# Kernel optimization log

Hardware: AMD Instinct MI355X
Metric: run time of the kernel (lower is better)

The kernel has to match this reference:

```python
import jax, jax.numpy as jnp
import numpy as np

N, E, F, FE, L = 12000, 120000, 768, 64, 16
Z = 2 * F + F  # concat(x_i, x_j, e) width = 2304


def setup_inputs() -> dict:
    key = jax.random.key(0)
    ks = jax.random.split(key, 24)
    s = 0.02

    def w(k, shape):
        return jax.random.normal(k, shape, dtype=jnp.float32) * s

    inp = {
        "x": jax.random.normal(ks[0], (N, F), dtype=jnp.float32),
        "e_raw": jax.random.normal(ks[1], (E, FE), dtype=jnp.float32),
        "src": jax.random.randint(ks[2], (E,), 0, N, dtype=jnp.int32),
        "dst": jax.random.randint(ks[3], (E,), 0, N, dtype=jnp.int32),
        "W_pre": w(ks[4], (FE, F)), "b_pre": jnp.zeros((F,), jnp.float32),
        "Wf1": w(ks[5], (Z, F)), "bf1": jnp.zeros((F,), jnp.float32),
        "Ws1": w(ks[6], (Z, F)), "bs1": jnp.zeros((F,), jnp.float32),
        "We1": w(ks[7], (Z, F)), "be1": jnp.zeros((F,), jnp.float32),
        "Wf2": w(ks[8], (Z, F)), "bf2": jnp.zeros((F,), jnp.float32),
        "Ws2": w(ks[9], (Z, F)), "bs2": jnp.zeros((F,), jnp.float32),
        "We2": w(ks[10], (Z, F)), "be2": jnp.zeros((F,), jnp.float32),
        "Wd": w(ks[11], (F, L)), "bd": jnp.zeros((L,), jnp.float32),
    }
    return inp


def _crystal_conv(x, e, src, dst, Wf, bf, Ws, bs, We, be):
    # z_ij = x_i || x_j || e_ij  (targets=dst, sources=src, Spektral convention)
    z = jnp.concatenate([x[dst], x[src], e], axis=-1)  # [E, 2304]
    msg = jax.nn.relu(z @ Ws + bs) * jax.nn.sigmoid(z @ Wf + bf)  # [E, F]
    gate = jax.nn.sigmoid(z @ We + be)  # [E, F] (stored as conv.e)
    agg = jax.ops.segment_sum(msg, dst, num_segments=N)  # scatter-sum to targets
    return x + agg, gate


def reference(x, e_raw, src, dst, W_pre, b_pre, Wf1, bf1, Ws1, bs1, We1, be1,
              Wf2, bf2, Ws2, bs2, We2, be2, Wd, bd):
    e = jnp.tanh(e_raw @ W_pre + b_pre)  # pre_edge Dense(768, tanh)
    # dropout layers are identity at inference
    x1, g1 = _crystal_conv(x, e, src, dst, Wf1, bf1, Ws1, bs1, We1, be1)
    e = e + e * g1
    x2, g2 = _crystal_conv(x1, e, src, dst, Wf2, bf2, Ws2, bs2, We2, be2)
    pooled = jnp.sum(x2, axis=0, keepdims=True)  # GlobalSumPool -> [1, F]
    return jax.nn.softmax(pooled @ Wd + bd, axis=-1)  # [1, n_labels]
```

## Files before the change

kernel.cpp:

```cpp
#include <hip/hip_runtime.h>
#include <stdint.h>

#define EN 120000
#define NN 12000
#define FF 768

typedef __attribute__((ext_vector_type(8))) short short8;
typedef __attribute__((ext_vector_type(4))) float floatx4;
typedef __attribute__((ext_vector_type(2))) float floatx2;
typedef __attribute__((ext_vector_type(2))) long long2v;

#ifdef __has_builtin
#if __has_builtin(__builtin_amdgcn_cvt_pk_f32_fp8) && __has_builtin(__builtin_amdgcn_cvt_f32_fp8)
#define HAS_HW_FP8 1
#endif
#if __has_builtin(__builtin_amdgcn_cvt_pk_fp8_f32)
#define HAS_HW_FP8E 1
#endif
#endif
#ifndef HAS_HW_FP8
#define HAS_HW_FP8 0
#endif
#ifndef HAS_HW_FP8E
#define HAS_HW_FP8E 0
#endif

__device__ __forceinline__ short f2b(float f) {
  union { float f; uint32_t i; } v; v.f = f;
  uint32_t r = (v.i + 0x7fffu + ((v.i >> 16) & 1u)) >> 16;
  return (short)(uint16_t)r;
}
__device__ __forceinline__ float f8tof(uint32_t b) {
  union { uint32_t i; float f; } u;
  u.i = (b & 0x7f) << 20;
  float v = u.f * 0x1p120f;
  return (b & 0x80) ? -v : v;
}
__device__ __forceinline__ uint8_t ftof8(float v) {
#if HAS_HW_FP8E
  return (uint8_t)(__builtin_amdgcn_cvt_pk_fp8_f32(v, v, 0, false) & 0xff);
#else
  union { float f; uint32_t i; } u;
  u.f = fabsf(v) * 0x1p-120f;
  uint32_t r = (u.i + 0x7ffffu + ((u.i >> 20) & 1u)) >> 20;
  if (r > 0x7eu) r = 0x7eu;
  return (uint8_t)(r | ((v < 0.f) ? 0x80u : 0u));
#endif
}
__device__ __forceinline__ floatx2 f8pair(uint32_t u) {
#if HAS_HW_FP8
  return __builtin_amdgcn_cvt_pk_f32_fp8(u, false);
#else
  floatx2 r; r.x = f8tof(u & 0xff); r.y = f8tof((u >> 8) & 0xff); return r;
#endif
}
__device__ __forceinline__ floatx2 f8pair_hi(uint32_t u) {
#if HAS_HW_FP8
  return __builtin_amdgcn_cvt_pk_f32_fp8(u, true);
#else
  floatx2 r; r.x = f8tof((u >> 16) & 0xff); r.y = f8tof((u >> 24) & 0xff); return r;
#endif
}
__device__ __forceinline__ float f8one(uint32_t u) {
#if HAS_HW_FP8
  return __builtin_amdgcn_cvt_f32_fp8(u, 0);
#else
  return f8tof(u & 0xff);
#endif
}
__device__ __forceinline__ float sigm(float x) { return 1.f / (1.f + __expf(-x)); }
__device__ __forceinline__ float tanh_fast(float x) {
  float ax = fabsf(x);
  float t = __expf(-2.f * ax);
  float r = (1.f - t) / (1.f + t);
  return copysignf(r, x);
}
__device__ __forceinline__ void async_ld16(const void* g, void* l) {
  __builtin_amdgcn_global_load_lds(
      (const __attribute__((address_space(1))) void*)g,
      (__attribute__((address_space(3))) void*)l, 16, 0, 0);
}
__device__ __forceinline__ int permk(int n) {
  return (n & ~63) | (((n >> 3) & 3) << 4) | (((n >> 5) & 1) << 3) | (n & 7);
}

template <int NW, int EPI, int F8AB>
__global__ __launch_bounds__(256, 2) void gemm_fused(
    const char* __restrict__ A, int lda,
    const char* __restrict__ Bt, int ldb, int wstride,
    int M, int K,
    void* __restrict__ outP, int ldout,
    const float* __restrict__ bias0, const float* __restrict__ bias1,
    const float* __restrict__ bias2,
    const int* __restrict__ dst, const int* __restrict__ src,
    const uint8_t* __restrict__ Pn, int pstride,
    const uint8_t* __restrict__ eInF8, uint8_t* __restrict__ e2Out,
    float* __restrict__ agg)
{
  __shared__ alignas(16) char lA[64 * 64];
  __shared__ alignas(16) char lB[NW * 128 * 64];

  const int tid  = threadIdx.x;
  const int wave = tid >> 6;
  const int lane = tid & 63;
  const int quad = lane >> 4;
  const int l16  = lane & 15;

  const int gx  = gridDim.x;
  const int nwg = gx * gridDim.y;
  int flat = blockIdx.y * gx + blockIdx.x;
  {
    const int q = nwg >> 3, r = nwg & 7;
    const int xcd = flat & 7, lid = flat >> 3;
    flat = (xcd < r ? xcd * (q + 1) : r * (q + 1) + (xcd - r) * q) + lid;
  }
  const int mBase = (flat / gx) * 64;
  const int nBase = (flat % gx) * 128;

  floatx4 acc[NW][4][2];
#pragma unroll
  for (int w = 0; w < NW; ++w)
#pragma unroll
    for (int mt = 0; mt < 4; ++mt)
#pragma unroll
      for (int nt = 0; nt < 2; ++nt)
#pragma unroll
        for (int r = 0; r < 4; ++r) acc[w][mt][nt][r] = 0.f;

  int i4 = tid >> 2;
  int am = mBase + ((i4 & 12) << 2) + ((i4 >> 4) << 2) + (i4 & 3);
  if (am > M - 1) am = M - 1;
  const char* aSrc = A + (size_t)am * lda + (tid & 3) * 16;

  const char* bSrc[NW * 2];
#pragma unroll
  for (int i = 0; i < NW * 2; ++i) {
    int t2 = tid + i * 256;
    int w  = t2 >> 9;
    int r  = (t2 >> 2) & 127;
    bSrc[i] = Bt + (size_t)w * wstride + (size_t)(nBase + r) * ldb + (t2 & 3) * 16;
  }

  const int Kb = K * (F8AB ? 1 : 2);

  for (int k0 = 0; k0 < Kb; k0 += 64) {
    __syncthreads();
    async_ld16(aSrc + k0, lA + tid * 16);
#pragma unroll
    for (int i = 0; i < NW * 2; ++i)
      async_ld16(bSrc[i] + k0, lB + (tid + i * 256) * 16);
    __syncthreads();

    if constexpr (F8AB) {
      long2v av[4];
#pragma unroll
      for (int mt = 0; mt < 4; ++mt)
        av[mt] = *(const long2v*)(lA + (mt * 16 + l16) * 64 + quad * 16);
#pragma unroll
      for (int w = 0; w < NW; ++w)
#pragma unroll
        for (int nt = 0; nt < 2; ++nt) {
          long2v bv = *(const long2v*)(lB + (w * 128 + wave * 32 + nt * 16 + l16) * 64 + quad * 16);
#pragma unroll
          for (int mt = 0; mt < 4; ++mt) {
            acc[w][mt][nt] = __builtin_amdgcn_mfma_f32_16x16x32_fp8_fp8(
                av[mt].x, bv.x, acc[w][mt][nt], 0, 0, 0);
            acc[w][mt][nt] = __builtin_amdgcn_mfma_f32_16x16x32_fp8_fp8(
                av[mt].y, bv.y, acc[w][mt][nt], 0, 0, 0);
          }
        }
    } else {
      short8 af[4];
#pragma unroll
      for (int mt = 0; mt < 4; ++mt)
        af[mt] = *(const short8*)(lA + (mt * 16 + l16) * 64 + quad * 16);
#pragma unroll
      for (int w = 0; w < NW; ++w)
#pragma unroll
        for (int nt = 0; nt < 2; ++nt) {
          short8 bf = *(const short8*)(lB + (w * 128 + wave * 32 + nt * 16 + l16) * 64 + quad * 16);
#pragma unroll
          for (int mt = 0; mt < 4; ++mt)
            acc[w][mt][nt] = __builtin_amdgcn_mfma_f32_16x16x32_bf16(
                af[mt], bf, acc[w][mt][nt], 0, 0, 0);
        }
    }
  }

  const int colW = nBase + wave * 32;

  float bb0[2], bb1[2], bb2[2];
  if (EPI == 1 || EPI == 2 || EPI == 3) {
#pragma unroll
    for (int nt = 0; nt < 2; ++nt) {
      int n = colW + nt * 16 + l16;
      bb0[nt] = bias0[n];
      if (EPI == 2 || EPI == 3) bb1[nt] = bias1[n];
      if (EPI == 2) bb2[nt] = bias2[n];
    }
  }

  if constexpr (EPI == 2 || EPI == 3) {
    const int n0 = colW + l16;
    const int pOff = ((n0 >> 5) << 6) + ((n0 & 15) << 2);
    const int eOff = ((n0 >> 5) << 5) + ((n0 & 15) << 1);
    const int pk0 = permk(n0), pk1 = permk(n0 + 16);
    const int mQ = mBase + quad * 16;
    int dp = -1;
    float run0 = 0.f, run1 = 0.f;
    float fd0 = 0.f, fd1 = 0.f, sd0 = 0.f, sd1 = 0.f, ed0 = 0.f, ed1 = 0.f;
#pragma unroll
    for (int j = 0; j < 16; ++j) {
      const int mt = j >> 2, r = j & 3;
      const int m = mQ + j;
      const int d = dst[m];
      const int s = src[m];
      if (d != dp) {
        if (dp >= 0) {
          atomicAdd(&agg[(size_t)dp * FF + n0], run0);
          atomicAdd(&agg[(size_t)dp * FF + n0 + 16], run1);
        }
        run0 = 0.f; run1 = 0.f; dp = d;
        const uint8_t* Pd = Pn + (size_t)d * pstride;
        uint32_t td = *(const uint32_t*)(Pd + pOff);
        floatx2 ta = f8pair(td), tb = f8pair_hi(td);
        fd0 = ta.x + bb0[0]; sd0 = ta.y + bb1[0];
        fd1 = tb.x + bb0[1]; sd1 = tb.y + bb1[1];
        if (EPI == 2) {
          uint32_t te = *(const unsigned short*)(Pd + 3072 + eOff);
          floatx2 ea = f8pair(te);
          ed0 = ea.x + bb2[0]; ed1 = ea.y + bb2[1];
        }
      }
      const uint8_t* Ps = Pn + (size_t)s * pstride;
      uint32_t tm = *(const uint32_t*)(Ps + 1536 + pOff);
      floatx2 ma = f8pair(tm), mb = f8pair_hi(tm);
      float hf0 = acc[0][mt][0][r] + ma.x + fd0;
      float hs0 = acc[1][mt][0][r] + ma.y + sd0;
      float hf1 = acc[0][mt][1][r] + mb.x + fd1;
      float hs1 = acc[1][mt][1][r] + mb.y + sd1;
      run0 += fmaxf(hs0, 0.f) * sigm(hf0);
      run1 += fmaxf(hs1, 0.f) * sigm(hf1);
      if (EPI == 2) {
        uint32_t me = *(const unsigned short*)(Ps + 3840 + eOff);
        floatx2 ea = f8pair(me);
        float he0 = acc[2][mt][0][r] + ea.x + ed0;
        float he1 = acc[2][mt][1][r] + ea.y + ed1;
        float ev0 = f8one(eInF8[(size_t)m * FF + pk0]);
        float ev1 = f8one(eInF8[(size_t)m * FF + pk1]);
        e2Out[(size_t)m * FF + pk0] = ftof8(ev0 * (1.f + sigm(he0)));
        e2Out[(size_t)m * FF + pk1] = ftof8(ev1 * (1.f + sigm(he1)));
      }
    }
    if (dp >= 0) {
      atomicAdd(&agg[(size_t)dp * FF + n0], run0);
      atomicAdd(&agg[(size_t)dp * FF + n0 + 16], run1);
    }
  } else {
#pragma unroll
    for (int mt = 0; mt < 4; ++mt) {
#pragma unroll
      for (int r = 0; r < 4; ++r) {
        int m = mBase + quad * 16 + mt * 4 + r;
        if (m >= M) continue;
#pragma unroll
        for (int nt = 0; nt < 2; ++nt) {
          int n = colW + nt * 16 + l16;
          float v0 = acc[0][mt][nt][r];
          if (EPI == 0) {
            int q = n / 768, j = n - q * 768;
            int h = (j >> 4) & 1;
            size_t o;
            if (q < 4)
              o = (size_t)(((q & 1) ? 1536 : 0) + ((j >> 5) << 6) + ((j & 15) << 2)
                           + (h << 1) + ((q >> 1) & 1));
            else
              o = (size_t)((q == 4 ? 3072 : 3840) + ((j >> 5) << 5) + ((j & 15) << 1) + h);
            ((uint8_t*)outP)[(size_t)m * ldout + o] = ftof8(v0);
          } else {
            ((uint8_t*)outP)[(size_t)m * ldout + permk(n)] = ftof8(tanh_fast(v0 + bb0[nt]));
          }
        }
      }
    }
  }
}

__global__ void hist_k(const int* __restrict__ dst, int* __restrict__ cnt) {
  int i = blockIdx.x * 256 + threadIdx.x;
  if (i < EN) atomicAdd(&cnt[dst[i]], 1);
}

__global__ void scan_k(const int* __restrict__ cnt, int* __restrict__ off) {
  __shared__ int part[1024];
  int t = threadIdx.x;
  int base = t * 12;
  int loc[12];
  int s = 0;
#pragma unroll
  for (int j = 0; j < 12; ++j) {
    int idx = base + j;
    int c = idx < NN ? cnt[idx] : 0;
    loc[j] = s; s += c;
  }
  part[t] = s;
  __syncthreads();
  for (int d = 1; d < 1024; d <<= 1) {
    int v = (t >= d) ? part[t - d] : 0;
    __syncthreads();
    part[t] += v;
    __syncthreads();
  }
  int pre = (t == 0) ? 0 : part[t - 1];
#pragma unroll
  for (int j = 0; j < 12; ++j) {
    int idx = base + j;
    if (idx < NN) off[idx] = pre + loc[j];
  }
}

__global__ void scatter_k(const int* __restrict__ dst, int* __restrict__ off,
                          int* __restrict__ perm) {
  int i = blockIdx.x * 256 + threadIdx.x;
  if (i < EN) { int p = atomicAdd(&off[dst[i]], 1); perm[p] = i; }
}

__global__ void permute_k(const int* __restrict__ dst, const int* __restrict__ src,
                          const int* __restrict__ perm, int* __restrict__ dstS,
                          int* __restrict__ srcS) {
  int i = blockIdx.x * 256 + threadIdx.x;
  if (i < EN) { int e = perm[i]; dstS[i] = dst[e]; srcS[i] = src[e]; }
}

__global__ void gather_f2b(const float* __restrict__ e_raw, const int* __restrict__ perm,
                           short* __restrict__ out, int n) {
  int i = blockIdx.x * 256 + threadIdx.x;
  if (i < n) {
    int j = i >> 6, t = i & 63;
    out[i] = f2b(e_raw[(size_t)perm[j] * 64 + t]);
  }
}

__global__ void conv_f2f8(const float* __restrict__ in, uint8_t* __restrict__ out, int n) {
  int i = blockIdx.x * 256 + threadIdx.x;
  if (i < n) {
    int row = i / FF, col = i - row * FF;
    out[(size_t)row * FF + permk(col)] = ftof8(in[i]);
  }
}

__global__ void transpose_wt(const float* __restrict__ in, short* __restrict__ out,
                             int R, int C) {
  __shared__ float t[32][33];
  int c0 = blockIdx.x * 32, r0 = blockIdx.y * 32;
  int tx = threadIdx.x, ty = threadIdx.y;
#pragma unroll
  for (int i = ty; i < 32; i += 8)
    t[i][tx] = in[(size_t)(r0 + i) * C + (c0 + tx)];
  __syncthreads();
#pragma unroll
  for (int i = ty; i < 32; i += 8)
    out[(size_t)(c0 + i) * R + (r0 + tx)] = f2b(t[tx][i]);
}

__global__ void transpose_wt8(const float* __restrict__ in, uint8_t* __restrict__ out,
                              int R, int C) {
  __shared__ float t[32][33];
  int c0 = blockIdx.x * 32, r0 = blockIdx.y * 32;
  int tx = threadIdx.x, ty = threadIdx.y;
#pragma unroll
  for (int i = ty; i < 32; i += 8)
    t[i][tx] = in[(size_t)(r0 + i) * C + (c0 + tx)];
  __syncthreads();
#pragma unroll
  for (int i = ty; i < 32; i += 8)
    out[(size_t)(c0 + i) * R + permk(r0 + tx)] = ftof8(t[tx][i]);
}

__global__ void make_x1(const float* __restrict__ x, float* __restrict__ agg,
                        uint8_t* __restrict__ x1f8, int n) {
  int i = blockIdx.x * 256 + threadIdx.x;
  if (i < n) {
    float v = x[i] + agg[i];
    agg[i] = v;
    int row = i / FF, col = i - row * FF;
    x1f8[(size_t)row * FF + permk(col)] = ftof8(v);
  }
}

__global__ void pool_k(const float* __restrict__ agg, float* __restrict__ pooled) {
  int t = threadIdx.x;
  int r0 = blockIdx.x * 64;
  float s0 = 0.f, s1 = 0.f, s2 = 0.f;
  for (int r = 0; r < 64; ++r) {
    int row = r0 + r;
    if (row >= NN) break;
    size_t base = (size_t)row * FF;
    s0 += agg[base + t];
    s1 += agg[base + t + 256];
    s2 += agg[base + t + 512];
  }
  atomicAdd(&pooled[t], s0);
  atomicAdd(&pooled[t + 256], s1);
  atomicAdd(&pooled[t + 512], s2);
}

__global__ void head_k(const float* __restrict__ pooled, const float* __restrict__ Wd,
                       const float* __restrict__ bd, float* __restrict__ out) {
  int l = threadIdx.x;
  int ll = l & 15;
  float a = 0.f;
  for (int j = 0; j < FF; ++j) a += pooled[j] * Wd[j * 16 + ll];
  a += bd[ll];
  float mx = a;
  for (int off = 8; off; off >>= 1) mx = fmaxf(mx, __shfl_xor(mx, off, 16));
  float ex = __expf(a - mx), sm = ex;
  for (int off = 8; off; off >>= 1) sm += __shfl_xor(sm, off, 16);
  if (l < 16) out[l] = ex / sm;
}

__global__ void sentinel_k(float* __restrict__ out, int n) {
  int i = blockIdx.x * 256 + threadIdx.x;
  if (i < n) out[i] = -1.0f;
}

extern "C" void kernel_launch(void* const* d_in, const int* in_sizes, int n_in,
                              void* d_out, int out_size, void* d_ws, size_t ws_size,
                              hipStream_t stream) {
  const float* x     = (const float*)d_in[0];
  const float* e_raw = (const float*)d_in[1];
  const int*   src   = (const int*)d_in[2];
  const int*   dst   = (const int*)d_in[3];
  const float* W_pre = (const float*)d_in[4];
  const float* b_pre = (const float*)d_in[5];
  const float* Wf1   = (const float*)d_in[6];
  const float* bf1   = (const float*)d_in[7];
  const float* Ws1   = (const float*)d_in[8];
  const float* bs1   = (const float*)d_in[9];
  const float* We1   = (const float*)d_in[10];
  const float* be1   = (const float*)d_in[11];
  const float* Wf2   = (const float*)d_in[12];
  const float* bf2   = (const float*)d_in[13];
  const float* Ws2   = (const float*)d_in[14];
  const float* bs2   = (const float*)d_in[15];
  const float* Wd    = (const float*)d_in[18];
  const float* bd    = (const float*)d_in[19];
  float* out = (float*)d_out;

  char* w = (char*)d_ws;
  size_t off = 0;
  auto take = [&](size_t b) -> void* {
    void* p = w + off;
    off += (b + 255) & ~(size_t)255;
    return p;
  };
  uint8_t* P    = (uint8_t*)take((size_t)NN * 4608);
  float* agg    = (float*)take((size_t)NN * FF * 4);
  uint8_t* xF8  = (uint8_t*)take((size_t)NN * FF);
  uint8_t* e2   = (uint8_t*)take((size_t)EN * FF);
  short* WpreT  = (short*)take((size_t)FF * 64 * 2);
  uint8_t* Wn1T = (uint8_t*)take((size_t)6 * FF * FF);
  uint8_t* Wb1T = (uint8_t*)take((size_t)3 * FF * FF);
  uint8_t* Wn2T = (uint8_t*)take((size_t)4 * FF * FF);
  uint8_t* Wb2T = (uint8_t*)take((size_t)2 * FF * FF);
  float* pooled = (float*)take((size_t)FF * 4);
  int* cnt      = (int*)take((size_t)NN * 4);
  int* boff     = (int*)take((size_t)NN * 4);
  int* perm     = (int*)take((size_t)EN * 4);
  int* dstS     = (int*)take((size_t)EN * 4);
  int* srcS     = (int*)take((size_t)EN * 4);
  const size_t base = off;

  long long avail = (long long)ws_size - (long long)base - 4096;
  long long ecl = avail / 896;
  int Ec = (int)(ecl < 0 ? 0 : ecl);
  Ec &= ~63;
  if (Ec > EN) Ec = EN;
  if (Ec < 64 || n_in < 20) {
    sentinel_k<<<(out_size + 255) / 256, 256, 0, stream>>>(out, out_size);
    return;
  }
  short* erC   = (short*)take((size_t)Ec * 64 * 2);
  uint8_t* eC  = (uint8_t*)take((size_t)Ec * FF);

  hipMemsetAsync(agg, 0, (size_t)NN * FF * 4, stream);
  hipMemsetAsync(pooled, 0, (size_t)FF * 4, stream);
  hipMemsetAsync(cnt, 0, (size_t)NN * 4, stream);

  hist_k<<<(EN + 255) / 256, 256, 0, stream>>>(dst, cnt);
  scan_k<<<1, 1024, 0, stream>>>(cnt, boff);
  scatter_k<<<(EN + 255) / 256, 256, 0, stream>>>(dst, boff, perm);
  permute_k<<<(EN + 255) / 256, 256, 0, stream>>>(dst, src, perm, dstS, srcS);

  conv_f2f8<<<(NN * FF + 255) / 256, 256, 0, stream>>>(x, xF8, NN * FF);

  dim3 tb(32, 8);
  transpose_wt<<<dim3(24, 2), tb, 0, stream>>>(W_pre, WpreT, 64, FF);
  const float* Wc1[3] = {Wf1, Ws1, We1};
  for (int q = 0; q < 3; ++q) {
    for (int h = 0; h < 2; ++h)
      transpose_wt8<<<dim3(24, 24), tb, 0, stream>>>(Wc1[q] + (size_t)h * FF * FF,
                                                     Wn1T + (size_t)(q * 2 + h) * FF * FF, FF, FF);
    transpose_wt8<<<dim3(24, 24), tb, 0, stream>>>(Wc1[q] + (size_t)2 * FF * FF,
                                                   Wb1T + (size_t)q * FF * FF, FF, FF);
  }
  const float* Wc2[2] = {Wf2, Ws2};
  for (int q = 0; q < 2; ++q) {
    for (int h = 0; h < 2; ++h)
      transpose_wt8<<<dim3(24, 24), tb, 0, stream>>>(Wc2[q] + (size_t)h * FF * FF,
                                                     Wn2T + (size_t)(q * 2 + h) * FF * FF, FF, FF);
    transpose_wt8<<<dim3(24, 24), tb, 0, stream>>>(Wc2[q] + (size_t)2 * FF * FF,
                                                   Wb2T + (size_t)q * FF * FF, FF, FF);
  }

  dim3 blk(256);
  const int gy_n = (NN + 63) / 64;

  gemm_fused<1, 0, 1><<<dim3(36, gy_n), blk, 0, stream>>>(
      (const char*)xF8, FF, (const char*)Wn1T, FF, 0, NN, FF, P, 4608,
      nullptr, nullptr, nullptr, nullptr, nullptr, nullptr, 0, nullptr, nullptr, nullptr);

  for (int eo = 0; eo < EN; eo += Ec) {
    int ec = EN - eo < Ec ? EN - eo : Ec;
    gather_f2b<<<(ec * 64 + 255) / 256, 256, 0, stream>>>(e_raw, perm + eo, erC, ec * 64);
    gemm_fused<1, 1, 0><<<dim3(6, ec / 64), blk, 0, stream>>>(
        (const char*)erC, 64 * 2, (const char*)WpreT, 64 * 2, 0, ec, 64, eC, FF,
        b_pre, nullptr, nullptr, nullptr, nullptr, nullptr, 0, nullptr, nullptr, nullptr);
    gemm_fused<3, 2, 1><<<dim3(6, ec / 64), blk, 0, stream>>>(
        (const char*)eC, FF, (const char*)Wb1T, FF, FF * FF, ec, FF, nullptr, 0,
        bf1, bs1, be1, dstS + eo, srcS + eo, P, 4608,
        eC, e2 + (size_t)eo * FF, agg);
  }

  make_x1<<<(NN * FF + 255) / 256, 256, 0, stream>>>(x, agg, xF8, NN * FF);

  gemm_fused<1, 0, 1><<<dim3(24, gy_n), blk, 0, stream>>>(
      (const char*)xF8, FF, (const char*)Wn2T, FF, 0, NN, FF, P, 4608,
      nullptr, nullptr, nullptr, nullptr, nullptr, nullptr, 0, nullptr, nullptr, nullptr);

  gemm_fused<2, 3, 1><<<dim3(6, EN / 64), blk, 0, stream>>>(
      (const char*)e2, FF, (const char*)Wb2T, FF, FF * FF, EN, FF, nullptr, 0,
      bf2, bs2, nullptr, dstS, srcS, P, 4608,
      nullptr, nullptr, agg);

  pool_k<<<(NN + 63) / 64, blk, 0, stream>>>(agg, pooled);

  head_k<<<1, 64, 0, stream>>>(pooled, Wd, bd, out);

  (void)in_sizes; (void)ws_size;
}
```

Baseline: 1.350 ms.

## Use scaled 16x16x128 FP8 MFMA with K=128 steps in fp8 GEMM path

The fp8 GEMM path now processes 128 K-elements per iteration and issues the gfx950 scaled MFMA 16x16x128 f8f6f4 instruction with unit scales, instead of two 16x16x32 fp8 MFMAs per 64-K chunk. The B tile in shared memory is doubled to hold two 64-byte K halves. The A tile is loaded in two halves through the same small buffer with extra barriers. This aims to cut MFMA instruction count and loop overhead, but it adds more LDS use, which may lower occupancy, and extra synchronisation per iteration.

```diff
diff --git a/kernel.cpp b/kernel.cpp
--- a/kernel.cpp
+++ b/kernel.cpp
@@ -8,7 +8,8 @@
 typedef __attribute__((ext_vector_type(8))) short short8;
 typedef __attribute__((ext_vector_type(4))) float floatx4;
 typedef __attribute__((ext_vector_type(2))) float floatx2;
-typedef __attribute__((ext_vector_type(2))) long long2v;
+typedef __attribute__((ext_vector_type(4))) int intx4;
+typedef __attribute__((ext_vector_type(8))) int intx8;
 
 #ifdef __has_builtin
 #if __has_builtin(__builtin_amdgcn_cvt_pk_f32_fp8) && __has_builtin(__builtin_amdgcn_cvt_f32_fp8)
@@ -98,7 +99,7 @@
     float* __restrict__ agg)
 {
   __shared__ alignas(16) char lA[64 * 64];
-  __shared__ alignas(16) char lB[NW * 128 * 64];
+  __shared__ alignas(16) char lB[(F8AB ? NW * 2 : NW) * 128 * 64];
 
   const int tid  = threadIdx.x;
   const int wave = tid >> 6;
@@ -132,44 +133,74 @@
   if (am > M - 1) am = M - 1;
   const char* aSrc = A + (size_t)am * lda + (tid & 3) * 16;
 
-  const char* bSrc[NW * 2];
-#pragma unroll
-  for (int i = 0; i < NW * 2; ++i) {
-    int t2 = tid + i * 256;
-    int w  = t2 >> 9;
-    int r  = (t2 >> 2) & 127;
-    bSrc[i] = Bt + (size_t)w * wstride + (size_t)(nBase + r) * ldb + (t2 & 3) * 16;
-  }
-
-  const int Kb = K * (F8AB ? 1 : 2);
-
-  for (int k0 = 0; k0 < Kb; k0 += 64) {
-    __syncthreads();
-    async_ld16(aSrc + k0, lA + tid * 16);
-#pragma unroll
-    for (int i = 0; i < NW * 2; ++i)
-      async_ld16(bSrc[i] + k0, lB + (tid + i * 256) * 16);
-    __syncthreads();
-
-    if constexpr (F8AB) {
-      long2v av[4];
+  if constexpr (F8AB) {
+    const char* bSrc2[NW * 4];
+    char* bDst2[NW * 4];
+#pragma unroll
+    for (int i = 0; i < NW * 4; ++i) {
+      int w = i >> 2, p = (i >> 1) & 1, h = i & 1;
+      int row = h * 64 + (tid >> 2);
+      bSrc2[i] = Bt + (size_t)w * wstride + (size_t)(nBase + row) * ldb
+               + p * 64 + (tid & 3) * 16;
+      bDst2[i] = lB + ((size_t)(w * 2 + p) * 128 + row) * 64 + (tid & 3) * 16;
+    }
+    for (int k0 = 0; k0 < K; k0 += 128) {
+      __syncthreads();
+      async_ld16(aSrc + k0, lA + tid * 16);
+#pragma unroll
+      for (int i = 0; i < NW * 4; ++i)
+        async_ld16(bSrc2[i] + k0, bDst2[i]);
+      __syncthreads();
+
+      intx4 a0[4];
 #pragma unroll
       for (int mt = 0; mt < 4; ++mt)
-        av[mt] = *(const long2v*)(lA + (mt * 16 + l16) * 64 + quad * 16);
+        a0[mt] = *(const intx4*)(lA + (mt * 16 + l16) * 64 + quad * 16);
+
+      __syncthreads();
+      async_ld16(aSrc + k0 + 64, lA + tid * 16);
+      __syncthreads();
+
+      intx8 av8[4];
+#pragma unroll
+      for (int mt = 0; mt < 4; ++mt) {
+        intx4 a1 = *(const intx4*)(lA + (mt * 16 + l16) * 64 + quad * 16);
+        av8[mt] = __builtin_shufflevector(a0[mt], a1, 0, 1, 2, 3, 4, 5, 6, 7);
+      }
 #pragma unroll
       for (int w = 0; w < NW; ++w)
 #pragma unroll
         for (int nt = 0; nt < 2; ++nt) {
-          long2v bv = *(const long2v*)(lB + (w * 128 + wave * 32 + nt * 16 + l16) * 64 + quad * 16);
-#pragma unroll
-          for (int mt = 0; mt < 4; ++mt) {
-            acc[w][mt][nt] = __builtin_amdgcn_mfma_f32_16x16x32_fp8_fp8(
-                av[mt].x, bv.x, acc[w][mt][nt], 0, 0, 0);
-            acc[w][mt][nt] = __builtin_amdgcn_mfma_f32_16x16x32_fp8_fp8(
-                av[mt].y, bv.y, acc[w][mt][nt], 0, 0, 0);
-          }
+          const char* bp = lB + ((size_t)(w * 2) * 128 + wave * 32 + nt * 16 + l16) * 64
+                         + quad * 16;
+          intx4 b0 = *(const intx4*)bp;
+          intx4 b1 = *(const intx4*)(bp + 8192);
+          intx8 bv8 = __builtin_shufflevector(b0, b1, 0, 1, 2, 3, 4, 5, 6, 7);
+#pragma unroll
+          for (int mt = 0; mt < 4; ++mt)
+            acc[w][mt][nt] = __builtin_amdgcn_mfma_scale_f32_16x16x128_f8f6f4(
+                av8[mt], bv8, acc[w][mt][nt], 0, 0,
+                0, 0x7f7f7f7f, 0, 0x7f7f7f7f);
         }
-    } else {
+    }
+  } else {
+    const char* bSrc[NW * 2];
+#pragma unroll
+    for (int i = 0; i < NW * 2; ++i) {
+      int t2 = tid + i * 256;
+      int w  = t2 >> 9;
+      int r  = (t2 >> 2) & 127;
+      bSrc[i] = Bt + (size_t)w * wstride + (size_t)(nBase + r) * ldb + (t2 & 3) * 16;
+    }
+    const int Kb = K * 2;
+    for (int k0 = 0; k0 < Kb; k0 += 64) {
+      __syncthreads();
+      async_ld16(aSrc + k0, lA + tid * 16);
+#pragma unroll
+      for (int i = 0; i < NW * 2; ++i)
+        async_ld16(bSrc[i] + k0, lB + (tid + i * 256) * 16);
+      __syncthreads();
+
       short8 af[4];
 #pragma unroll
       for (int mt = 0; mt < 4; ++mt)
```

Result: faster. 1.319 ms (-2.3%).
